# Kernel tuning notes

Hardware: AMD Instinct MI355X
Metric: run time of the kernel (lower is better)

Reference implementation:

```python
import jax, jax.numpy as jnp
import numpy as np

B, N, D, FH, FW, C = 4, 6, 41, 16, 44, 64
OGH, OGW = 256, 704           # final_dim; downsample=16 -> FH=16, FW=44
NX, NY, NZ = 200, 200, 1      # BEV grid from x/y/zbound
DX = jnp.array([0.5, 0.5, 20.0], dtype=jnp.float32)
BX = jnp.array([-49.75, -49.75, 0.0], dtype=jnp.float32)  # bound lo + dx/2


def make_frustum():
    # (D, FH, FW, 3) of (u_pixel, v_pixel, depth)
    ds = jnp.broadcast_to(jnp.linspace(2.0, 42.0, D)[:, None, None], (D, FH, FW))
    xs = jnp.broadcast_to(jnp.linspace(0.0, OGW - 1.0, FW)[None, None, :], (D, FH, FW))
    ys = jnp.broadcast_to(jnp.linspace(0.0, OGH - 1.0, FH)[None, :, None], (D, FH, FW))
    return jnp.stack([xs, ys, ds], axis=-1).astype(jnp.float32)


def setup_inputs() -> dict:
    key = jax.random.key(0)
    kx, kt = jax.random.split(key)
    x = jax.random.normal(kx, (B, N, D, FH, FW, C), dtype=jnp.float32)
    # camera->ego base rotation: cam z (forward) -> ego x, cam x (right) -> -ego y, cam y (down) -> -ego z
    base = np.array([[0.0, 0.0, 1.0], [-1.0, 0.0, 0.0], [0.0, -1.0, 0.0]], dtype=np.float32)
    rots = np.zeros((B, N, 3, 3), dtype=np.float32)
    for n in range(N):
        th = 2.0 * np.pi * n / N
        c, s = np.cos(th), np.sin(th)
        rz = np.array([[c, -s, 0.0], [s, c, 0.0], [0.0, 0.0, 1.0]], dtype=np.float32)
        rots[:, n] = rz @ base
    trans = 0.5 * jax.random.normal(kt, (B, N, 3), dtype=jnp.float32)
    intr = np.zeros((B, N, 3, 3), dtype=np.float32)
    intr[:, :, 0, 0] = 500.0
    intr[:, :, 1, 1] = 500.0
    intr[:, :, 0, 2] = OGW / 2.0
    intr[:, :, 1, 2] = OGH / 2.0
    intr[:, :, 2, 2] = 1.0
    post_rots = np.broadcast_to(np.eye(3, dtype=np.float32), (B, N, 3, 3)).copy()
    post_trans = np.zeros((B, N, 3), dtype=np.float32)
    return {"x": x, "rots": jnp.asarray(rots), "trans": trans,
            "intrins": jnp.asarray(intr), "post_rots": jnp.asarray(post_rots),
            "post_trans": jnp.asarray(post_trans)}


def get_geometry(rots, trans, intrins, post_rots, post_trans):
    frustum = make_frustum()                                   # (D,FH,FW,3)
    pts = frustum[None, None] - post_trans[:, :, None, None, None, :]
    pts = jnp.einsum('bnij,bndhwj->bndhwi', jnp.linalg.inv(post_rots), pts)
    # undo perspective: (u*d, v*d, d)
    pts = jnp.concatenate([pts[..., :2] * pts[..., 2:3], pts[..., 2:3]], axis=-1)
    combine = rots @ jnp.linalg.inv(intrins)                   # (B,N,3,3)
    pts = jnp.einsum('bnij,bndhwj->bndhwi', combine, pts)
    return pts + trans[:, :, None, None, None, :]              # (B,N,D,FH,FW,3)


def voxel_pooling(geom, x):
    Nprime = B * N * D * FH * FW
    feats = x.reshape(Nprime, C)
    # quantize to voxel indices (torch .long() truncates toward zero)
    g = ((geom - (BX - DX / 2.0)) / DX).astype(jnp.int32).reshape(Nprime, 3)
    batch_ix = jnp.repeat(jnp.arange(B, dtype=jnp.int32), Nprime // B)
    kept = ((g[:, 0] >= 0) & (g[:, 0] < NX) & (g[:, 1] >= 0) & (g[:, 1] < NY)
            & (g[:, 2] >= 0) & (g[:, 2] < NZ))
    # flat index over (B, NZ, NY, NX); invalid points contribute zeros to voxel 0
    idx = ((batch_ix * NZ + g[:, 2]) * NY + g[:, 1]) * NX + g[:, 0]
    idx = jnp.where(kept, idx, 0)
    feats = jnp.where(kept[:, None], feats, 0.0)
    grid = jnp.zeros((B * NZ * NY * NX, C), dtype=feats.dtype).at[idx].add(feats)
    grid = grid.reshape(B, NZ, NY, NX, C).transpose(0, 1, 4, 2, 3)  # (B,NZ,C,NY,NX)
    return grid.reshape(B, NZ * C, NY, NX)  # == torch.cat(unbind(dim=2), 1)


def reference(x, rots, trans, intrins, post_rots, post_trans):
    geom = get_geometry(rots, trans, intrins, post_rots, post_trans)
    return voxel_pooling(geom, x)
```

## Files before the change

kernel.cpp:

```cpp
#include <hip/hip_runtime.h>
#include <hip/hip_bf16.h>

namespace {
constexpr int B = 4, N = 6, D = 41, FH = 16, FW = 44, C = 64;
constexpr int NX = 200, NY = 200;
constexpr int NGROUPS = B * N * D * FW;
constexpr long long ACC_ELEMS = (long long)B * NY * NX * C;
constexpr int PARAMS_PER_CAM = 24;
constexpr int FLAG_IDX = B * N * PARAMS_PER_CAM;
constexpr int CTR_OFF = 640;
constexpr int SEG_OFF = 704;
}

__device__ __forceinline__ float ldin(const void* p, size_t idx, int fp32m) {
  return fp32m ? ((const float*)p)[idx]
               : __bfloat162float(((const __hip_bfloat16*)p)[idx]);
}

__device__ __forceinline__ float dot3(float m0, float m1, float m2, float a0,
                                      float a1, float a2) {
  return __fadd_rn(__fadd_rn(__fmul_rn(m0, a0), __fmul_rn(m1, a1)),
                   __fmul_rn(m2, a2));
}

__device__ __forceinline__ int voxel_of(const float* pr, float ax, float az,
                                        int b, int h) {
  float v = (float)(17 * h);
  float ay = __fsub_rn(v, pr[10]);
  float qx = dot3(pr[0], pr[1], pr[2], ax, ay, az);
  float qy = dot3(pr[3], pr[4], pr[5], ax, ay, az);
  float qz = dot3(pr[6], pr[7], pr[8], ax, ay, az);
  qx = __fmul_rn(qx, qz);
  qy = __fmul_rn(qy, qz);
  float gx = __fadd_rn(dot3(pr[12], pr[13], pr[14], qx, qy, qz), pr[21]);
  float gy = __fadd_rn(dot3(pr[15], pr[16], pr[17], qx, qy, qz), pr[22]);
  float gz = __fadd_rn(dot3(pr[18], pr[19], pr[20], qx, qy, qz), pr[23]);
  int ix = (int)__fdiv_rn(__fsub_rn(gx, -50.0f), 0.5f);
  int iy = (int)__fdiv_rn(__fsub_rn(gy, -50.0f), 0.5f);
  int iz = (int)__fdiv_rn(__fsub_rn(gz, -10.0f), 20.0f);
  if (ix >= 0 && ix < NX && iy >= 0 && iy < NY && iz == 0)
    return (b * NY + iy) * NX + ix;
  return -1;
}

__device__ inline void inv3x3_f64(const float a_[9], float o[9]) {
  double a[9];
  for (int k = 0; k < 9; ++k) a[k] = (double)a_[k];
  double c00 = a[4] * a[8] - a[5] * a[7];
  double c01 = a[5] * a[6] - a[3] * a[8];
  double c02 = a[3] * a[7] - a[4] * a[6];
  double det = a[0] * c00 + a[1] * c01 + a[2] * c02;
  double id = 1.0 / det;
  o[0] = (float)(c00 * id);
  o[1] = (float)((a[2] * a[7] - a[1] * a[8]) * id);
  o[2] = (float)((a[1] * a[5] - a[2] * a[4]) * id);
  o[3] = (float)(c01 * id);
  o[4] = (float)((a[0] * a[8] - a[2] * a[6]) * id);
  o[5] = (float)((a[2] * a[3] - a[0] * a[5]) * id);
  o[6] = (float)(c02 * id);
  o[7] = (float)((a[1] * a[6] - a[0] * a[7]) * id);
  o[8] = (float)((a[0] * a[4] - a[1] * a[3]) * id);
}

__global__ void setup_kernel(const void* rots, const void* trans,
                             const void* intr, const void* prots,
                             const void* ptrans, float* params) {
  int i = threadIdx.x;
  float probe = ((const float*)intr)[0];
  int fp32m = (probe > 100.f && probe < 2000.f) ? 1 : 0;
  if (i == 0) {
    ((int*)params)[FLAG_IDX] = fp32m;
    ((int*)params)[CTR_OFF] = 0;
  }
  if (i >= B * N) return;
  float R[9], K[9], PR[9];
  for (int k = 0; k < 9; ++k) {
    R[k] = ldin(rots, (size_t)i * 9 + k, fp32m);
    K[k] = ldin(intr, (size_t)i * 9 + k, fp32m);
    PR[k] = ldin(prots, (size_t)i * 9 + k, fp32m);
  }
  float iPR[9];
  inv3x3_f64(PR, iPR);
  float i00 = __fdiv_rn(1.f, K[0]);
  float i11 = __fdiv_rn(1.f, K[4]);
  float i22 = __fdiv_rn(1.f, K[8]);
  float i01 = __fmul_rn(-i11, __fmul_rn(i00, K[1]));
  float x1 = __fmul_rn(i00, K[2]);
  x1 = __fadd_rn(x1, __fmul_rn(K[5], i01));
  float x2 = __fmul_rn(i11, K[5]);
  float i02 = __fmul_rn(-i22, x1);
  float i12 = __fmul_rn(-i22, x2);
  float iK[9] = {i00, i01, i02, 0.f, i11, i12, 0.f, 0.f, i22};
  float* o = params + i * PARAMS_PER_CAM;
  for (int k = 0; k < 9; ++k) o[k] = iPR[k];
  for (int k = 0; k < 3; ++k) o[9 + k] = ldin(ptrans, (size_t)i * 3 + k, fp32m);
  for (int r = 0; r < 3; ++r)
    for (int c2 = 0; c2 < 3; ++c2)
      o[12 + r * 3 + c2] = dot3(R[r * 3], R[r * 3 + 1], R[r * 3 + 2], iK[c2],
                                iK[3 + c2], iK[6 + c2]);
  for (int k = 0; k < 3; ++k) o[21 + k] = ldin(trans, (size_t)i * 3 + k, fp32m);
}

__global__ void zero_kernel(float4* __restrict__ acc, int n4) {
  int i = blockIdx.x * blockDim.x + threadIdx.x;
  if (i < n4) acc[i] = make_float4(0.f, 0.f, 0.f, 0.f);
}

__global__ __launch_bounds__(256) void geom_kernel(float* params) {
  int g = blockIdx.x * blockDim.x + threadIdx.x;
  int lane = threadIdx.x & 63;
  int* counter = (int*)params + CTR_OFF;
  int2* segs = (int2*)((int*)params + SEG_OFF);
  int nseg = 0;
  const float* pr = nullptr;
  float ax = 0.f, az = 0.f;
  int b = 0;
  if (g < NGROUPS) {
    int w = g % FW;
    int t = g / FW;
    int d = t % D;
    t /= D;
    int n = t % N;
    b = t / N;
    pr = params + (b * N + n) * PARAMS_PER_CAM;
    float u = (w == FW - 1) ? 703.0f : (float)((double)w * (703.0 / 43.0));
    float dep = (float)(2 + d);
    ax = __fsub_rn(u, pr[9]);
    az = __fsub_rn(dep, pr[11]);
    int curvox = -1;
    for (int h = 0; h < FH; ++h) {
      int vox = voxel_of(pr, ax, az, b, h);
      if (vox >= 0 && vox != curvox) {
        ++nseg;
        curvox = vox;
      }
    }
  }
  int incl = nseg;
#pragma unroll
  for (int s = 1; s < 64; s <<= 1) {
    int y = __shfl_up(incl, s, 64);
    if (lane >= s) incl += y;
  }
  int total = __shfl(incl, 63, 64);
  int excl = incl - nseg;
  int basev = 0;
  if (lane == 63 && total > 0) basev = atomicAdd(counter, total);
  basev = __shfl(basev, 63, 64);
  if (g < NGROUPS && nseg > 0) {
    int curvox = -1, mask = 0, k = 0;
    for (int h = 0; h < FH; ++h) {
      int vox = voxel_of(pr, ax, az, b, h);
      if (vox >= 0) {
        if (vox != curvox) {
          if (curvox >= 0) {
            segs[basev + excl + k] = make_int2((g << 16) | mask, curvox);
            ++k;
          }
          curvox = vox;
          mask = 0;
        }
        mask |= (1 << h);
      }
    }
    if (curvox >= 0)
      segs[basev + excl + k] = make_int2((g << 16) | mask, curvox);
  }
}

__global__ __launch_bounds__(256) void gather_kernel(
    const void* __restrict__ x, const float* __restrict__ params,
    float* __restrict__ acc) {
  int lane = threadIdx.x & 63;
  int wid = blockIdx.x * (blockDim.x >> 6) + (threadIdx.x >> 6);
  int nwaves = gridDim.x * (blockDim.x >> 6);
  int total = ((const int*)params)[CTR_OFF];
  int fp32m = ((const int*)params)[FLAG_IDX];
  const int2* segs = (const int2*)((const int*)params + SEG_OFF);
  for (int s = wid; s < total; s += nwaves) {
    int2 e = segs[s];
    int g = ((unsigned)e.x) >> 16;
    int mask = e.x & 0xffff;
    int vox = e.y;
    int w = g % FW;
    int t = g / FW;
    size_t base = ((size_t)t * FH * FW + w) * (size_t)C + lane;
    float v[FH];
#pragma unroll
    for (int h = 0; h < FH; ++h)
      v[h] = ((mask >> h) & 1) ? ldin(x, base + (size_t)(h * FW * C), fp32m)
                               : 0.0f;
    float sum = v[0];
#pragma unroll
    for (int h = 1; h < FH; ++h) sum = __fadd_rn(sum, v[h]);
    atomicAdd(acc + (size_t)vox * C + lane, sum);
  }
}

__global__ __launch_bounds__(256) void finalize_kernel(
    const float* __restrict__ acc, void* __restrict__ out,
    const float* __restrict__ params) {
  int fp32m = ((const int*)params)[FLAG_IDX];
  int y = blockIdx.x % NY;
  int b = blockIdx.x / NY;
  __shared__ float tile[NX * 65];
  const float4* src = (const float4*)(acc + (size_t)(b * NY + y) * NX * C);
  for (int i = threadIdx.x; i < NX * 16; i += 256) {
    float4 vv = src[i];
    int xx = i >> 4, c4 = i & 15;
    float* dst = &tile[xx * 65 + c4 * 4];
    dst[0] = vv.x;
    dst[1] = vv.y;
    dst[2] = vv.z;
    dst[3] = vv.w;
  }
  __syncthreads();
  for (int i = threadIdx.x; i < C * (NX / 4); i += 256) {
    int cc = i / (NX / 4), k = i % (NX / 4);
    int xx = 4 * k;
    float4 vv;
    vv.x = tile[xx * 65 + cc];
    vv.y = tile[(xx + 1) * 65 + cc];
    vv.z = tile[(xx + 2) * 65 + cc];
    vv.w = tile[(xx + 3) * 65 + cc];
    size_t o = ((size_t)(b * C + cc) * NY + y) * NX + xx;
    if (fp32m) {
      *(float4*)((float*)out + o) = vv;
    } else {
      __hip_bfloat16* op = (__hip_bfloat16*)out + o;
      op[0] = __float2bfloat16(vv.x);
      op[1] = __float2bfloat16(vv.y);
      op[2] = __float2bfloat16(vv.z);
      op[3] = __float2bfloat16(vv.w);
    }
  }
}

extern "C" void kernel_launch(void* const* d_in, const int* in_sizes, int n_in,
                              void* d_out, int out_size, void* d_ws,
                              size_t ws_size, hipStream_t stream) {
  const void* x = d_in[0];
  const void* rots = d_in[1];
  const void* trans = d_in[2];
  const void* intr = d_in[3];
  const void* prots = d_in[4];
  const void* ptrans = d_in[5];

  float* acc = (float*)d_ws;
  float* params = acc + ACC_ELEMS;

  setup_kernel<<<1, 64, 0, stream>>>(rots, trans, intr, prots, ptrans, params);

  int n4 = (int)(ACC_ELEMS / 4);
  zero_kernel<<<(n4 + 255) / 256, 256, 0, stream>>>((float4*)acc, n4);

  geom_kernel<<<(NGROUPS + 255) / 256, 256, 0, stream>>>(params);

  gather_kernel<<<16384, 256, 0, stream>>>(x, params, acc);

  finalize_kernel<<<B * NY, 256, 0, stream>>>(acc, d_out, params);
}
```

Measured before the change: 311.0 us.

## Zero only touched voxels via per-voxel flags and fold camera setup into geom

Drops the full zeroing of the roughly 41 MB accumulator. A new pass zeroes only the voxels named by segments and sets a per-voxel byte flag. Finalize reads the accumulator only where the flag is set and writes zeros elsewhere. The separate setup kernel is removed: each geom block recomputes the camera parameters into shared memory, and the fp32 probe is redone in every kernel. This trades a large memset for an extra scattered pass and redundant per-block setup work.

```diff
diff --git a/kernel.cpp b/kernel.cpp
--- a/kernel.cpp
+++ b/kernel.cpp
@@ -6,15 +6,22 @@
 constexpr int NX = 200, NY = 200;
 constexpr int NGROUPS = B * N * D * FW;
 constexpr long long ACC_ELEMS = (long long)B * NY * NX * C;
+constexpr int NVOX = B * NY * NX;
 constexpr int PARAMS_PER_CAM = 24;
-constexpr int FLAG_IDX = B * N * PARAMS_PER_CAM;
-constexpr int CTR_OFF = 640;
-constexpr int SEG_OFF = 704;
+constexpr size_t CTR_BYTE = (size_t)ACC_ELEMS * 4;
+constexpr size_t FLAG_BYTE = CTR_BYTE + 4;
+constexpr size_t SEG_BYTE = 41120008;
+constexpr int ZINIT_DWORDS = (4 + NVOX + 3) / 4;
 }
 
 __device__ __forceinline__ float ldin(const void* p, size_t idx, int fp32m) {
   return fp32m ? ((const float*)p)[idx]
                : __bfloat162float(((const __hip_bfloat16*)p)[idx]);
+}
+
+__device__ __forceinline__ int probe_fp32(const void* intr) {
+  float probe = ((const float*)intr)[0];
+  return (probe > 100.f && probe < 2000.f) ? 1 : 0;
 }
 
 __device__ __forceinline__ float dot3(float m0, float m1, float m2, float a0,
@@ -62,17 +69,9 @@
   o[8] = (float)((a[0] * a[4] - a[1] * a[3]) * id);
 }
 
-__global__ void setup_kernel(const void* rots, const void* trans,
-                             const void* intr, const void* prots,
-                             const void* ptrans, float* params) {
-  int i = threadIdx.x;
-  float probe = ((const float*)intr)[0];
-  int fp32m = (probe > 100.f && probe < 2000.f) ? 1 : 0;
-  if (i == 0) {
-    ((int*)params)[FLAG_IDX] = fp32m;
-    ((int*)params)[CTR_OFF] = 0;
-  }
-  if (i >= B * N) return;
+__device__ void compute_cam_params(int i, const void* rots, const void* trans,
+                                   const void* intr, const void* prots,
+                                   const void* ptrans, int fp32m, float* o) {
   float R[9], K[9], PR[9];
   for (int k = 0; k < 9; ++k) {
     R[k] = ldin(rots, (size_t)i * 9 + k, fp32m);
@@ -91,7 +90,6 @@
   float i02 = __fmul_rn(-i22, x1);
   float i12 = __fmul_rn(-i22, x2);
   float iK[9] = {i00, i01, i02, 0.f, i11, i12, 0.f, 0.f, i22};
-  float* o = params + i * PARAMS_PER_CAM;
   for (int k = 0; k < 9; ++k) o[k] = iPR[k];
   for (int k = 0; k < 3; ++k) o[9 + k] = ldin(ptrans, (size_t)i * 3 + k, fp32m);
   for (int r = 0; r < 3; ++r)
@@ -101,16 +99,27 @@
   for (int k = 0; k < 3; ++k) o[21 + k] = ldin(trans, (size_t)i * 3 + k, fp32m);
 }
 
-__global__ void zero_kernel(float4* __restrict__ acc, int n4) {
+__global__ void zinit_kernel(char* __restrict__ ws) {
   int i = blockIdx.x * blockDim.x + threadIdx.x;
-  if (i < n4) acc[i] = make_float4(0.f, 0.f, 0.f, 0.f);
-}
-
-__global__ __launch_bounds__(256) void geom_kernel(float* params) {
+  if (i < ZINIT_DWORDS) ((int*)(ws + CTR_BYTE))[i] = 0;
+}
+
+__global__ __launch_bounds__(256) void geom_kernel(const void* rots,
+                                                   const void* trans,
+                                                   const void* intr,
+                                                   const void* prots,
+                                                   const void* ptrans,
+                                                   char* __restrict__ ws) {
+  __shared__ float sp[B * N * PARAMS_PER_CAM];
+  int fp32m = probe_fp32(intr);
+  if (threadIdx.x < B * N)
+    compute_cam_params(threadIdx.x, rots, trans, intr, prots, ptrans, fp32m,
+                       sp + threadIdx.x * PARAMS_PER_CAM);
+  __syncthreads();
   int g = blockIdx.x * blockDim.x + threadIdx.x;
   int lane = threadIdx.x & 63;
-  int* counter = (int*)params + CTR_OFF;
-  int2* segs = (int2*)((int*)params + SEG_OFF);
+  int* counter = (int*)(ws + CTR_BYTE);
+  int2* segs = (int2*)(ws + SEG_BYTE);
   int nseg = 0;
   const float* pr = nullptr;
   float ax = 0.f, az = 0.f;
@@ -122,7 +131,7 @@
     t /= D;
     int n = t % N;
     b = t / N;
-    pr = params + (b * N + n) * PARAMS_PER_CAM;
+    pr = sp + (b * N + n) * PARAMS_PER_CAM;
     float u = (w == FW - 1) ? 703.0f : (float)((double)w * (703.0 / 43.0));
     float dep = (float)(2 + d);
     ax = __fsub_rn(u, pr[9]);
@@ -168,15 +177,31 @@
   }
 }
 
-__global__ __launch_bounds__(256) void gather_kernel(
-    const void* __restrict__ x, const float* __restrict__ params,
-    float* __restrict__ acc) {
+__global__ __launch_bounds__(256) void zseg_kernel(char* __restrict__ ws) {
   int lane = threadIdx.x & 63;
   int wid = blockIdx.x * (blockDim.x >> 6) + (threadIdx.x >> 6);
   int nwaves = gridDim.x * (blockDim.x >> 6);
-  int total = ((const int*)params)[CTR_OFF];
-  int fp32m = ((const int*)params)[FLAG_IDX];
-  const int2* segs = (const int2*)((const int*)params + SEG_OFF);
+  int total = *(const int*)(ws + CTR_BYTE);
+  const int2* segs = (const int2*)(ws + SEG_BYTE);
+  float* acc = (float*)ws;
+  unsigned char* flags = (unsigned char*)(ws + FLAG_BYTE);
+  for (int s = wid; s < total; s += nwaves) {
+    int vox = segs[s].y;
+    acc[(size_t)vox * C + lane] = 0.0f;
+    if (lane == 0) flags[vox] = 1;
+  }
+}
+
+__global__ __launch_bounds__(256) void gather_kernel(const void* __restrict__ x,
+                                                     const void* intr,
+                                                     char* __restrict__ ws) {
+  int lane = threadIdx.x & 63;
+  int wid = blockIdx.x * (blockDim.x >> 6) + (threadIdx.x >> 6);
+  int nwaves = gridDim.x * (blockDim.x >> 6);
+  int total = *(const int*)(ws + CTR_BYTE);
+  int fp32m = probe_fp32(intr);
+  const int2* segs = (const int2*)(ws + SEG_BYTE);
+  float* acc = (float*)ws;
   for (int s = wid; s < total; s += nwaves) {
     int2 e = segs[s];
     int g = ((unsigned)e.x) >> 16;
@@ -198,16 +223,18 @@
 }
 
 __global__ __launch_bounds__(256) void finalize_kernel(
-    const float* __restrict__ acc, void* __restrict__ out,
-    const float* __restrict__ params) {
-  int fp32m = ((const int*)params)[FLAG_IDX];
+    const char* __restrict__ ws, void* __restrict__ out, const void* intr) {
+  int fp32m = probe_fp32(intr);
   int y = blockIdx.x % NY;
   int b = blockIdx.x / NY;
+  const float* acc = (const float*)ws;
+  const unsigned char* flg =
+      (const unsigned char*)(ws + FLAG_BYTE) + (size_t)(b * NY + y) * NX;
   __shared__ float tile[NX * 65];
   const float4* src = (const float4*)(acc + (size_t)(b * NY + y) * NX * C);
   for (int i = threadIdx.x; i < NX * 16; i += 256) {
-    float4 vv = src[i];
     int xx = i >> 4, c4 = i & 15;
+    float4 vv = flg[xx] ? src[i] : make_float4(0.f, 0.f, 0.f, 0.f);
     float* dst = &tile[xx * 65 + c4 * 4];
     dst[0] = vv.x;
     dst[1] = vv.y;
@@ -245,18 +272,16 @@
   const void* intr = d_in[3];
   const void* prots = d_in[4];
   const void* ptrans = d_in[5];
-
-  float* acc = (float*)d_ws;
-  float* params = acc + ACC_ELEMS;
-
-  setup_kernel<<<1, 64, 0, stream>>>(rots, trans, intr, prots, ptrans, params);
-
-  int n4 = (int)(ACC_ELEMS / 4);
-  zero_kernel<<<(n4 + 255) / 256, 256, 0, stream>>>((float4*)acc, n4);
-
-  geom_kernel<<<(NGROUPS + 255) / 256, 256, 0, stream>>>(params);
-
-  gather_kernel<<<16384, 256, 0, stream>>>(x, params, acc);
-
-  finalize_kernel<<<B * NY, 256, 0, stream>>>(acc, d_out, params);
-}
+  char* ws = (char*)d_ws;
+
+  zinit_kernel<<<(ZINIT_DWORDS + 255) / 256, 256, 0, stream>>>(ws);
+
+  geom_kernel<<<(NGROUPS + 255) / 256, 256, 0, stream>>>(rots, trans, intr,
+                                                         prots, ptrans, ws);
+
+  zseg_kernel<<<4096, 256, 0, stream>>>(ws);
+
+  gather_kernel<<<16384, 256, 0, stream>>>(x, intr, ws);
+
+  finalize_kernel<<<B * NY, 256, 0, stream>>>(ws, d_out, intr);
+}
```

Measured after the change: 302.7 us. -2.6%, faster.
